# Performance work log

Hardware: AMD Instinct MI355X
Metric: run time of the kernel (lower is better)

The kernel has to match this reference:

```python
import jax, jax.numpy as jnp
import numpy as np

C = 512
HEADS = 8
HEAD_DIM = C // HEADS
GROUPS = 32
EPS = 1e-5


def group_norm(x, scale, bias):
    b, c, h, w = x.shape
    xg = x.reshape(b, GROUPS, -1)
    mean = xg.mean(axis=-1, keepdims=True)
    var = xg.var(axis=-1, keepdims=True)
    xg = (xg - mean) * jax.lax.rsqrt(var + EPS)
    x = xg.reshape(b, c, h, w)
    return x * scale[None, :, None, None] + bias[None, :, None, None]


def conv1x1(x, w, b):
    # w: (out_c, in_c), x: (B, C, H, W)
    return jnp.einsum('oc,bchw->bohw', w, x) + b[None, :, None, None]


def setup_inputs() -> dict:
    key = jax.random.key(0)
    ks = jax.random.split(key, 11)
    s = 1.0 / np.sqrt(C)
    return {
        'x': jax.random.normal(ks[0], (8, C, 32, 32), jnp.float32),
        'gn_scale': jnp.ones((C,), jnp.float32),
        'gn_bias': jnp.zeros((C,), jnp.float32),
        'wq': jax.random.normal(ks[1], (C, C), jnp.float32) * s,
        'bq': jax.random.normal(ks[2], (C,), jnp.float32) * 0.01,
        'wk': jax.random.normal(ks[3], (C, C), jnp.float32) * s,
        'bk': jax.random.normal(ks[4], (C,), jnp.float32) * 0.01,
        'wv': jax.random.normal(ks[5], (C, C), jnp.float32) * s,
        'bv': jax.random.normal(ks[6], (C,), jnp.float32) * 0.01,
        'wp': jax.random.normal(ks[7], (C, C), jnp.float32) * s,
        'bp': jax.random.normal(ks[8], (C,), jnp.float32) * 0.01,
    }


def reference(x, gn_scale, gn_bias, wq, bq, wk, bk, wv, bv, wp, bp):
    b, c, h, w = x.shape
    n = h * w
    h_in = x
    xn = group_norm(x, gn_scale, gn_bias)
    q = conv1x1(xn, wq, bq).reshape(b, HEADS, HEAD_DIM, n)
    k = conv1x1(xn, wk, bk).reshape(b, HEADS, HEAD_DIM, n)
    v = conv1x1(xn, wv, bv).reshape(b, HEADS, HEAD_DIM, n)
    scale = 1.0 / np.sqrt(HEAD_DIM).astype(np.float32)
    attn = jnp.einsum('bhcn,bhcm->bhnm', q, k) * scale
    attn = jax.nn.softmax(attn, axis=-1)
    out = jnp.einsum('bhnm,bhcm->bhcn', attn, v)
    out = out.reshape(b, c, h, w)
    out = conv1x1(out, wp, bp)
    return out + h_in
```

## Files before the change

kernel.cpp:

```cpp
#include <hip/hip_runtime.h>

#define CC 512
#define NN 1024
#define NB 8
#define NH 8
#define HD 64

typedef __attribute__((ext_vector_type(8))) short s16x8;
typedef __attribute__((ext_vector_type(4))) short s16x4;
typedef __attribute__((ext_vector_type(4))) float f32x4;
typedef __attribute__((ext_vector_type(16))) float f32x16;

__device__ __forceinline__ short f2bf(float f){
  union { float f; unsigned u; } v; v.f = f;
  unsigned r = v.u + 0x7fffu + ((v.u >> 16) & 1u);
  return (short)(r >> 16);
}

__device__ __forceinline__ unsigned cvtpk(float lo, float hi){
  unsigned r;
  asm("v_cvt_pk_bf16_f32 %0, %1, %2" : "=v"(r) : "v"(lo), "v"(hi));
  return r;
}

__device__ __forceinline__ void gload16(const void* g, void* l){
  __builtin_amdgcn_global_load_lds((const __attribute__((address_space(1))) void*)g,
                                   (__attribute__((address_space(3))) void*)l, 16, 0, 0);
}

__global__ __launch_bounds__(256) void wcvt(const float* __restrict__ w0, const float* __restrict__ w1,
    const float* __restrict__ w2, const float* __restrict__ w3, short* __restrict__ wbf){
  const int i = blockIdx.x*256 + threadIdx.x;
  const int sel = i >> 16;
  const int off = (i & 65535) << 2;
  const float* src = (sel==0) ? w0 : (sel==1) ? w1 : (sel==2) ? w2 : w3;
  const float4 v = *reinterpret_cast<const float4*>(src + off);
  s16x4 o;
  o[0] = f2bf(v.x); o[1] = f2bf(v.y); o[2] = f2bf(v.z); o[3] = f2bf(v.w);
  *reinterpret_cast<s16x4*>(wbf + (size_t)sel*262144 + off) = o;
}

__global__ __launch_bounds__(256) void gn_kernel(const float* __restrict__ x,
    const float* __restrict__ gsc, const float* __restrict__ gbi, short* __restrict__ xnt){
  const int b = blockIdx.x >> 5;
  const int g = blockIdx.x & 31;
  const int t = threadIdx.x;
  const float* base = x + ((size_t)b*CC + g*16)*NN;
  float4 vals[16];
  float s = 0.f, s2 = 0.f;
  #pragma unroll
  for (int k = 0; k < 16; ++k){
    float4 v = *reinterpret_cast<const float4*>(base + k*NN + t*4);
    vals[k] = v;
    s  += v.x + v.y + v.z + v.w;
    s2 += v.x*v.x + v.y*v.y + v.z*v.z + v.w*v.w;
  }
  #pragma unroll
  for (int m = 1; m < 64; m <<= 1){ s += __shfl_xor(s, m); s2 += __shfl_xor(s2, m); }
  __shared__ float rs[4], rs2[4];
  const int wid = t >> 6, lane = t & 63;
  if (lane == 0){ rs[wid] = s; rs2[wid] = s2; }
  __syncthreads();
  s  = rs[0] + rs[1] + rs[2] + rs[3];
  s2 = rs2[0] + rs2[1] + rs2[2] + rs2[3];
  const float mean = s * (1.f/16384.f);
  const float inv = rsqrtf(s2 * (1.f/16384.f) - mean*mean + 1e-5f);
  float scl[16], off[16];
  #pragma unroll
  for (int k = 0; k < 16; ++k){
    const float sc = gsc[g*16 + k] * inv;
    scl[k] = sc;
    off[k] = gbi[g*16 + k] - mean * sc;
  }
  short* obase = xnt + ((size_t)b*NN + t*4)*CC + g*16;
  #pragma unroll
  for (int i = 0; i < 4; ++i){
    s16x8 lo, hi;
    #pragma unroll
    for (int k = 0; k < 8; ++k){
      float v = (i==0) ? vals[k].x : (i==1) ? vals[k].y : (i==2) ? vals[k].z : vals[k].w;
      lo[k] = f2bf(v * scl[k] + off[k]);
    }
    #pragma unroll
    for (int k = 0; k < 8; ++k){
      float v = (i==0) ? vals[k+8].x : (i==1) ? vals[k+8].y : (i==2) ? vals[k+8].z : vals[k+8].w;
      hi[k] = f2bf(v * scl[k+8] + off[k+8]);
    }
    *reinterpret_cast<s16x8*>(obase + (size_t)i*CC)     = lo;
    *reinterpret_cast<s16x8*>(obase + (size_t)i*CC + 8) = hi;
  }
}

template<int MODE>
__global__ __launch_bounds__(256) void gemm_kernel(
    const short* __restrict__ Wb, const short* __restrict__ Bmat,
    const float* __restrict__ bias0, const float* __restrict__ bias1, const float* __restrict__ bias2,
    const float* __restrict__ resid,
    short* __restrict__ qt, short* __restrict__ kt2, short* __restrict__ vo,
    float* __restrict__ outp)
{
  const int tile = blockIdx.x;
  const int batch = blockIdx.y;
  const int z = blockIdx.z;
  const int mt = tile >> 3, nt = tile & 7;
  const int tid = threadIdx.x;
  const int lane = tid & 63, wid = tid >> 6;
  const int wm = wid >> 1, wn = wid & 1;

  __shared__ short As[128*64];
  __shared__ short Bs[128*64];

  const short* Wz = Wb + (size_t)(MODE == 0 ? z : 3) * 262144;
  const short* Brow = Bmat + ((size_t)batch*NN + nt*128)*CC;

  const f32x4 fzero = {0.f, 0.f, 0.f, 0.f};
  f32x4 acc[4][4];
  #pragma unroll
  for (int i = 0; i < 4; ++i)
  #pragma unroll
  for (int j = 0; j < 4; ++j)
    acc[i][j] = fzero;

  for (int kk = 0; kk < 8; ++kk){
    __syncthreads();
    #pragma unroll
    for (int j = 0; j < 4; ++j){
      const int id = tid + 256*j;
      const int row = id >> 3, ch = id & 7;
      const int gch = ch ^ (row & 7);
      gload16(Wz   + (size_t)(mt*128 + row)*CC + kk*64 + gch*8, As + (wid*64 + 256*j)*8);
      gload16(Brow + (size_t)row*CC          + kk*64 + gch*8, Bs + (wid*64 + 256*j)*8);
    }
    __syncthreads();
    #pragma unroll
    for (int ks = 0; ks < 2; ++ks){
      s16x8 a[4], b[4];
      #pragma unroll
      for (int mi = 0; mi < 4; ++mi){
        const int row = wm*64 + mi*16 + (lane & 15);
        const int ch = (ks*4 + (lane >> 4)) ^ (row & 7);
        a[mi] = *reinterpret_cast<const s16x8*>(&As[row*64 + ch*8]);
      }
      #pragma unroll
      for (int ni = 0; ni < 4; ++ni){
        const int row = wn*64 + ni*16 + (lane & 15);
        const int ch = (ks*4 + (lane >> 4)) ^ (row & 7);
        b[ni] = *reinterpret_cast<const s16x8*>(&Bs[row*64 + ch*8]);
      }
      if (MODE == 0 && z == 2){
        #pragma unroll
        for (int mi = 0; mi < 4; ++mi)
        #pragma unroll
        for (int ni = 0; ni < 4; ++ni)
          acc[mi][ni] = __builtin_amdgcn_mfma_f32_16x16x32_bf16(b[ni], a[mi], acc[mi][ni], 0, 0, 0);
      } else {
        #pragma unroll
        for (int mi = 0; mi < 4; ++mi)
        #pragma unroll
        for (int ni = 0; ni < 4; ++ni)
          acc[mi][ni] = __builtin_amdgcn_mfma_f32_16x16x32_bf16(a[mi], b[ni], acc[mi][ni], 0, 0, 0);
      }
    }
  }

  const int obase = mt*128 + wm*64;
  const int nbase = nt*128 + wn*64;
  if (MODE == 0){
    const int head = mt*2 + wm;
    const size_t hb = ((size_t)batch*NH + head)*65536;
    const int hi2 = (lane >> 5) & 1;
    const int j0 = ((lane >> 4) & 1)*4;
    if (z < 2){
      const float* bias = (z == 0) ? bias0 : bias1;
      short* dst = (z == 0) ? qt : kt2;
      const float qs = (z == 0) ? 0.125f * 1.44269504f : 1.0f;
      #pragma unroll
      for (int mi = 0; mi < 4; ++mi){
        float bv4[4];
        #pragma unroll
        for (int r = 0; r < 4; ++r) bv4[r] = bias[obase + mi*16 + (lane>>4)*4 + r];
        #pragma unroll
        for (int ni = 0; ni < 4; ++ni){
          const int l = (ni & 1)*16 + (lane & 15) + 32*hi2;
          const int q5 = nt*4 + wn*2 + (ni >> 1);
          s16x4 pk;
          #pragma unroll
          for (int r = 0; r < 4; ++r) pk[r] = f2bf((acc[mi][ni][r] + bv4[r]) * qs);
          *reinterpret_cast<s16x4*>(dst + hb + (size_t)((q5*4 + mi)*64 + l)*8 + j0) = pk;
        }
      }
    } else {
      #pragma unroll
      for (int mi = 0; mi < 4; ++mi){
        const float bv = bias2[obase + mi*16 + (lane & 15)];
        const int ci = mi >> 1;
        const int cl = (mi & 1)*16 + (lane & 15);
        #pragma unroll
        for (int ni = 0; ni < 4; ++ni){
          const int m5 = nt*2 + wn;
          s16x4 pk;
          #pragma unroll
          for (int r = 0; r < 4; ++r) pk[r] = f2bf(acc[mi][ni][r] + bv);
          *reinterpret_cast<s16x4*>(vo + hb + (size_t)((((ci*16 + m5)*4 + ni)*64) + cl + 32*hi2)*8 + j0) = pk;
        }
      }
    }
  } else {
    #pragma unroll
    for (int mi = 0; mi < 4; ++mi){
      float bv4[4];
      #pragma unroll
      for (int r = 0; r < 4; ++r) bv4[r] = bias0[obase + mi*16 + (lane>>4)*4 + r];
      #pragma unroll
      for (int ni = 0; ni < 4; ++ni){
        const int n = nbase + ni*16 + (lane & 15);
        #pragma unroll
        for (int r = 0; r < 4; ++r){
          const int o = obase + mi*16 + (lane>>4)*4 + r;
          const size_t idx = ((size_t)batch*CC + o)*NN + n;
          outp[idx] = acc[mi][ni][r] + bv4[r] + resid[idx];
        }
      }
    }
  }
}

__global__ __launch_bounds__(256, 2) void attn_kernel(
    const short* __restrict__ qp, const short* __restrict__ kp, const short* __restrict__ vp,
    short* __restrict__ ot)
{
  const int bid = blockIdx.x;
  const int xcd = bid & 7, rr = bid >> 3;
  const int bh  = xcd*8 + (rr & 7);
  const int qt  = rr >> 3;
  const int b = bh >> 3, head = bh & 7;
  const int tid = threadIdx.x, lane = tid & 63, wid = tid >> 6;
  const int col = lane & 31;
  const int qg = wid & 1, kh = wid >> 1;
  const int q0 = qt*64 + qg*32;

  const short* Qf = qp + (size_t)bh*65536;
  const short* Kf = kp + (size_t)bh*65536;
  const short* Vf = vp + (size_t)bh*65536;

  __shared__ float Lof[2][32][64];
  __shared__ float Lm[2][64];
  __shared__ float Ll[2][64];

  const int q5 = qt*2 + qg;
  s16x8 qf[4];
  #pragma unroll
  for (int ks = 0; ks < 4; ++ks)
    qf[ks] = *reinterpret_cast<const s16x8*>(Qf + (size_t)(q5*4 + ks)*512 + lane*8);

  f32x16 of0, of1;
  #pragma unroll
  for (int r = 0; r < 16; ++r){ of0[r] = 0.f; of1[r] = 0.f; }
  float m = -1e30f, l = 0.f;

  auto kload = [&](int itn, s16x8 (&kf)[2][4]){
    const short* kb = Kf + (size_t)(kh*16 + itn*2)*2048 + lane*8;
    #pragma unroll
    for (int t = 0; t < 2; ++t)
      #pragma unroll
      for (int ks = 0; ks < 4; ++ks)
        kf[t][ks] = *reinterpret_cast<const s16x8*>(kb + t*2048 + ks*512);
  };

  auto pack = [&](f32x16& sv, s16x8& p0, s16x8& p1){
    union { unsigned u[4]; s16x8 v; } w0, w1;
    {
      unsigned a = cvtpk(sv[0], sv[1]);
      unsigned c = cvtpk(sv[4], sv[5]);
      auto r = __builtin_amdgcn_permlane32_swap(a, c, false, false);
      w0.u[0] = r[0]; w0.u[2] = r[1];
      a = cvtpk(sv[2], sv[3]);
      c = cvtpk(sv[6], sv[7]);
      r = __builtin_amdgcn_permlane32_swap(a, c, false, false);
      w0.u[1] = r[0]; w0.u[3] = r[1];
    }
    {
      unsigned a = cvtpk(sv[8], sv[9]);
      unsigned c = cvtpk(sv[12], sv[13]);
      auto r = __builtin_amdgcn_permlane32_swap(a, c, false, false);
      w1.u[0] = r[0]; w1.u[2] = r[1];
      a = cvtpk(sv[10], sv[11]);
      c = cvtpk(sv[14], sv[15]);
      r = __builtin_amdgcn_permlane32_swap(a, c, false, false);
      w1.u[1] = r[0]; w1.u[3] = r[1];
    }
    p0 = w0.v; p1 = w1.v;
  };

  auto body = [&](int it, s16x8 (&kf)[2][4], s16x8 (&kfn)[2][4]){
    const int m5 = kh*8 + it;
    s16x8 vf[2][4];
    const short* vb = Vf + (size_t)m5*2048 + lane*8;
    #pragma unroll
    for (int ci = 0; ci < 2; ++ci)
      #pragma unroll
      for (int s = 0; s < 4; ++s)
        vf[ci][s] = *reinterpret_cast<const s16x8*>(vb + ci*32768 + s*512);
    f32x16 s0, s1;
    #pragma unroll
    for (int r = 0; r < 16; ++r){ s0[r] = 0.f; s1[r] = 0.f; }
    #pragma unroll
    for (int ks = 0; ks < 4; ++ks){
      s0 = __builtin_amdgcn_mfma_f32_32x32x16_bf16(kf[0][ks], qf[ks], s0, 0, 0, 0);
      s1 = __builtin_amdgcn_mfma_f32_32x32x16_bf16(kf[1][ks], qf[ks], s1, 0, 0, 0);
    }
    if (it < 7) kload(it + 1, kfn);
    float t[16];
    #pragma unroll
    for (int r = 0; r < 16; ++r) t[r] = fmaxf(s0[r], s1[r]);
    #pragma unroll
    for (int o = 8; o > 0; o >>= 1)
      #pragma unroll
      for (int r = 0; r < 8; ++r) if (r < o) t[r] = fmaxf(t[r], t[r + o]);
    float tm = fmaxf(t[0], __shfl_xor(t[0], 32));
    const float mn = fmaxf(m, tm);
    const float sc = __builtin_amdgcn_exp2f(m - mn);
    m = mn;
    #pragma unroll
    for (int r = 0; r < 16; ++r){ s0[r] = __builtin_amdgcn_exp2f(s0[r] - mn); }
    #pragma unroll
    for (int r = 0; r < 16; ++r){ s1[r] = __builtin_amdgcn_exp2f(s1[r] - mn); }
    #pragma unroll
    for (int r = 0; r < 16; ++r) t[r] = s0[r] + s1[r];
    #pragma unroll
    for (int o = 8; o > 0; o >>= 1)
      #pragma unroll
      for (int r = 0; r < 8; ++r) if (r < o) t[r] = t[r] + t[r + o];
    float rs = t[0] + __shfl_xor(t[0], 32);
    l = l*sc + rs;
    #pragma unroll
    for (int r = 0; r < 16; ++r){ of0[r] *= sc; of1[r] *= sc; }
    s16x8 pf[4];
    pack(s0, pf[0], pf[1]);
    pack(s1, pf[2], pf[3]);
    #pragma unroll
    for (int s = 0; s < 4; ++s){
      of0 = __builtin_amdgcn_mfma_f32_32x32x16_bf16(vf[0][s], pf[s], of0, 0, 0, 0);
      of1 = __builtin_amdgcn_mfma_f32_32x32x16_bf16(vf[1][s], pf[s], of1, 0, 0, 0);
    }
  };

  s16x8 kfA[2][4], kfB[2][4];
  kload(0, kfA);
  #pragma unroll 1
  for (int ii = 0; ii < 4; ++ii){
    body(2*ii,     kfA, kfB);
    body(2*ii + 1, kfB, kfA);
  }

  __syncthreads();
  if (kh == 1){
    #pragma unroll
    for (int r = 0; r < 16; ++r){
      Lof[qg][r][lane]      = of0[r];
      Lof[qg][16 + r][lane] = of1[r];
    }
    Lm[qg][lane] = m;
    Ll[qg][lane] = l;
  }
  __syncthreads();
  if (kh == 0){
    const float m1 = Lm[qg][lane], l1 = Ll[qg][lane];
    const float mn = fmaxf(m, m1);
    const float a0 = __builtin_amdgcn_exp2f(m - mn);
    const float a1 = __builtin_amdgcn_exp2f(m1 - mn);
    const float linv = 1.f / (l*a0 + l1*a1);
    const int hi = lane >> 5;
    const int n = q0 + col;
    short* ob = ot + ((size_t)b*NN + n)*CC + head*HD + hi*4;
    #pragma unroll
    for (int rq = 0; rq < 4; ++rq){
      s16x4 pk;
      #pragma unroll
      for (int r = 0; r < 4; ++r)
        pk[r] = f2bf((of0[rq*4 + r]*a0 + Lof[qg][rq*4 + r][lane]*a1) * linv);
      *reinterpret_cast<s16x4*>(ob + rq*8) = pk;
      #pragma unroll
      for (int r = 0; r < 4; ++r)
        pk[r] = f2bf((of1[rq*4 + r]*a0 + Lof[qg][16 + rq*4 + r][lane]*a1) * linv);
      *reinterpret_cast<s16x4*>(ob + 32 + rq*8) = pk;
    }
  }
}

extern "C" void kernel_launch(void* const* d_in, const int* in_sizes, int n_in,
                              void* d_out, int out_size, void* d_ws, size_t ws_size,
                              hipStream_t stream) {
  const float* x   = (const float*)d_in[0];
  const float* gsc = (const float*)d_in[1];
  const float* gbi = (const float*)d_in[2];
  const float* wq  = (const float*)d_in[3];
  const float* bq  = (const float*)d_in[4];
  const float* wk  = (const float*)d_in[5];
  const float* bk  = (const float*)d_in[6];
  const float* wv  = (const float*)d_in[7];
  const float* bv  = (const float*)d_in[8];
  const float* wp  = (const float*)d_in[9];
  const float* bp  = (const float*)d_in[10];
  float* out = (float*)d_out;

  char* ws = (char*)d_ws;
  short* wbf = (short*)(ws);
  short* xnt = (short*)(ws + (2u<<20));
  short* qt  = (short*)(ws + (10u<<20));
  short* kt  = (short*)(ws + (18u<<20));
  short* v   = (short*)(ws + (26u<<20));
  short* aot = (short*)(ws + (34u<<20));

  wcvt<<<1024, 256, 0, stream>>>(wq, wk, wv, wp, wbf);
  gn_kernel<<<256, 256, 0, stream>>>(x, gsc, gbi, xnt);
  gemm_kernel<0><<<dim3(32, 8, 3), 256, 0, stream>>>(wbf, xnt, bq, bk, bv, nullptr,
                                                     qt, kt, v, nullptr);
  attn_kernel<<<dim3(1024), 256, 0, stream>>>(qt, kt, v, aot);
  gemm_kernel<1><<<dim3(32, 8, 1), 256, 0, stream>>>(wbf, aot, bp, nullptr, nullptr, x,
                                                     nullptr, nullptr, nullptr, out);
}
```

Before: 84.23 us.

## Double-buffer GEMM LDS tiles and raise wave priority around attention MFMAs

After: 88.50 us. 1.05x slower.

```diff
diff --git a/kernel.cpp b/kernel.cpp
--- a/kernel.cpp
+++ b/kernel.cpp
@@ -107,8 +107,8 @@
   const int lane = tid & 63, wid = tid >> 6;
   const int wm = wid >> 1, wn = wid & 1;
 
-  __shared__ short As[128*64];
-  __shared__ short Bs[128*64];
+  __shared__ short As[2][128*64];
+  __shared__ short Bs[2][128*64];
 
   const short* Wz = Wb + (size_t)(MODE == 0 ? z : 3) * 262144;
   const short* Brow = Bmat + ((size_t)batch*NN + nt*128)*CC;
@@ -121,17 +121,19 @@
   for (int j = 0; j < 4; ++j)
     acc[i][j] = fzero;
 
-  for (int kk = 0; kk < 8; ++kk){
-    __syncthreads();
+  const int srow = tid >> 3, sch = tid & 7;
+  const int sgch = sch ^ (srow & 7);
+
+  auto stage = [&](int kk, int buf){
     #pragma unroll
     for (int j = 0; j < 4; ++j){
-      const int id = tid + 256*j;
-      const int row = id >> 3, ch = id & 7;
-      const int gch = ch ^ (row & 7);
-      gload16(Wz   + (size_t)(mt*128 + row)*CC + kk*64 + gch*8, As + (wid*64 + 256*j)*8);
-      gload16(Brow + (size_t)row*CC          + kk*64 + gch*8, Bs + (wid*64 + 256*j)*8);
-    }
-    __syncthreads();
+      const int row = srow + 32*j;
+      gload16(Wz   + (size_t)(mt*128 + row)*CC + kk*64 + sgch*8, &As[buf][(wid*64 + 256*j)*8]);
+      gload16(Brow + (size_t)row*CC            + kk*64 + sgch*8, &Bs[buf][(wid*64 + 256*j)*8]);
+    }
+  };
+
+  auto compute = [&](int buf){
     #pragma unroll
     for (int ks = 0; ks < 2; ++ks){
       s16x8 a[4], b[4];
@@ -139,13 +141,13 @@
       for (int mi = 0; mi < 4; ++mi){
         const int row = wm*64 + mi*16 + (lane & 15);
         const int ch = (ks*4 + (lane >> 4)) ^ (row & 7);
-        a[mi] = *reinterpret_cast<const s16x8*>(&As[row*64 + ch*8]);
+        a[mi] = *reinterpret_cast<const s16x8*>(&As[buf][row*64 + ch*8]);
       }
       #pragma unroll
       for (int ni = 0; ni < 4; ++ni){
         const int row = wn*64 + ni*16 + (lane & 15);
         const int ch = (ks*4 + (lane >> 4)) ^ (row & 7);
-        b[ni] = *reinterpret_cast<const s16x8*>(&Bs[row*64 + ch*8]);
+        b[ni] = *reinterpret_cast<const s16x8*>(&Bs[buf][row*64 + ch*8]);
       }
       if (MODE == 0 && z == 2){
         #pragma unroll
@@ -161,6 +163,18 @@
           acc[mi][ni] = __builtin_amdgcn_mfma_f32_16x16x32_bf16(a[mi], b[ni], acc[mi][ni], 0, 0, 0);
       }
     }
+  };
+
+  stage(0, 0);
+  __syncthreads();
+  #pragma unroll
+  for (int kk = 0; kk < 8; kk += 2){
+    if (kk + 1 < 8) stage(kk + 1, 1);
+    compute(0);
+    __syncthreads();
+    if (kk + 2 < 8) stage(kk + 2, 0);
+    compute(1);
+    __syncthreads();
   }
 
   const int obase = mt*128 + wm*64;
@@ -304,11 +318,13 @@
     f32x16 s0, s1;
     #pragma unroll
     for (int r = 0; r < 16; ++r){ s0[r] = 0.f; s1[r] = 0.f; }
+    __builtin_amdgcn_s_setprio(1);
     #pragma unroll
     for (int ks = 0; ks < 4; ++ks){
       s0 = __builtin_amdgcn_mfma_f32_32x32x16_bf16(kf[0][ks], qf[ks], s0, 0, 0, 0);
       s1 = __builtin_amdgcn_mfma_f32_32x32x16_bf16(kf[1][ks], qf[ks], s1, 0, 0, 0);
     }
+    __builtin_amdgcn_s_setprio(0);
     if (it < 7) kload(it + 1, kfn);
     float t[16];
     #pragma unroll
@@ -338,11 +354,13 @@
     s16x8 pf[4];
     pack(s0, pf[0], pf[1]);
     pack(s1, pf[2], pf[3]);
+    __builtin_amdgcn_s_setprio(1);
     #pragma unroll
     for (int s = 0; s < 4; ++s){
       of0 = __builtin_amdgcn_mfma_f32_32x32x16_bf16(vf[0][s], pf[s], of0, 0, 0, 0);
       of1 = __builtin_amdgcn_mfma_f32_32x32x16_bf16(vf[1][s], pf[s], of1, 0, 0, 0);
     }
+    __builtin_amdgcn_s_setprio(0);
   };
 
   s16x8 kfA[2][4], kfB[2][4];
```
